# Kernel tuning notes

Measured on AMD Instinct MI355X. Metric: run time of the kernel, lower is better.

## Reference

```python
import jax, jax.numpy as jnp
import numpy as np

B, N, H, V, STEP = 16, 50, 128, 40000, 2

def setup_inputs() -> dict:
    key = jax.random.key(0)
    ks = jax.random.split(key, 24)
    def nrm(i, shape, s=0.08):
        return jax.random.normal(ks[i], shape, jnp.float32) * s
    items = jax.random.randint(ks[0], (B, N), 0, V)
    A = jax.random.uniform(ks[1], (B, N, 2 * N), jnp.float32)
    lengths = jax.random.randint(ks[2], (B,), 1, N + 1)
    mask = (jnp.arange(N)[None, :] < lengths[:, None]).astype(jnp.int32)
    emb = nrm(3, (V, H), 0.1).at[0].set(0.0)  # padding_idx=0 row zeroed
    return dict(
        items=items, A=A, mask=mask, emb=emb,
        w_ih=nrm(4, (3 * H, 2 * H)), w_hh=nrm(5, (3 * H, H)),
        b_ih=nrm(6, (3 * H,)), b_hh=nrm(7, (3 * H,)),
        b_iah=nrm(8, (H,)), b_oah=nrm(9, (H,)),
        W_ein=nrm(10, (H, H)), b_ein=nrm(11, (H,)),
        W_eout=nrm(12, (H, H)), b_eout=nrm(13, (H,)),
        W_one=nrm(14, (H, H)), b_one=nrm(15, (H,)),
        W_two=nrm(16, (H, H)), b_two=nrm(17, (H,)),
        w_three=nrm(18, (H,)),
        W_tr=nrm(19, (H, 2 * H)), b_tr=nrm(20, (H,)),
        W_t=nrm(21, (H, H)),
    )

def gnn_cell(A, hidden, w_ih, w_hh, b_ih, b_hh, b_iah, b_oah, W_ein, b_ein, W_eout, b_eout):
    # A: [B,N,2N], hidden: [B,N,H]
    ein = hidden @ W_ein.T + b_ein
    eout = hidden @ W_eout.T + b_eout
    input_in = jnp.einsum('bnm,bmh->bnh', A[:, :, :N], ein) + b_iah
    input_out = jnp.einsum('bnm,bmh->bnh', A[:, :, N:], eout) + b_oah
    inputs = jnp.concatenate([input_in, input_out], axis=-1)  # [B,N,2H]
    gi = inputs @ w_ih.T + b_ih
    gh = hidden @ w_hh.T + b_hh
    i_r, i_i, i_n = jnp.split(gi, 3, axis=-1)
    h_r, h_i, h_n = jnp.split(gh, 3, axis=-1)
    resetgate = jax.nn.sigmoid(i_r + h_r)
    inputgate = jax.nn.sigmoid(i_i + h_i)
    newgate = jnp.tanh(i_n + resetgate * h_n)
    return newgate + inputgate * (hidden - newgate)

def reference(items, A, mask, emb, w_ih, w_hh, b_ih, b_hh, b_iah, b_oah,
              W_ein, b_ein, W_eout, b_eout, W_one, b_one, W_two, b_two,
              w_three, W_tr, b_tr, W_t):
    hidden = emb[items]  # [B,N,H]
    for _ in range(STEP):
        hidden = gnn_cell(A, hidden, w_ih, w_hh, b_ih, b_hh, b_iah, b_oah,
                          W_ein, b_ein, W_eout, b_eout)
    # compute_scores
    lengths = jnp.sum(mask, axis=1)  # all >= 1 by construction
    ht = hidden[jnp.arange(B), lengths - 1]  # [B,H] last valid item
    q1 = (ht @ W_one.T + b_one)[:, None, :]
    q2 = hidden @ W_two.T + b_two
    mexp = mask[..., None].astype(jnp.float32)  # [B,N,1]
    alpha_logits = jax.nn.sigmoid(q1 + q2) @ w_three[:, None]  # [B,N,1]
    alpha = jax.nn.softmax(jnp.where(mexp == 0, -jnp.inf, alpha_logits), axis=1)
    a = jnp.sum(alpha * hidden * mexp, axis=1)  # [B,H]
    a = jnp.concatenate([a, ht], axis=1) @ W_tr.T + b_tr  # hybrid (nonhybrid=False)
    b_emb = emb[1:]  # [V-1,H]
    qt = (hidden * mexp) @ W_t.T  # [B,N,H]
    beta_logits = jnp.einsum('vh,bnh->bvn', b_emb, qt)
    beta_logits = jnp.where(mask[:, None, :] == 0, -jnp.inf, beta_logits)
    beta = jax.nn.softmax(beta_logits, axis=-1)  # [B,V-1,N]
    target = jnp.einsum('bvn,bnh->bvh', beta, qt * mexp)  # [B,V-1,H]
    # scores = sum((a[:,None,:] + target) * b_emb, -1), split to avoid extra buffer
    scores = jnp.einsum('bvh,vh->bv', target, b_emb) + a @ b_emb.T
    return scores  # [B, V-1]
```

## Files before the change

### kernel.cpp

```cpp
#include <hip/hip_runtime.h>

#define BB 16
#define NN 50
#define HH 128
#define VV 40000
#define VO 39999

typedef unsigned short u16;
typedef unsigned int u32;
typedef __attribute__((ext_vector_type(8))) short short8;
typedef __attribute__((ext_vector_type(4))) float f32x4;

#define OFF_HID    0
#define OFF_EIN    102400
#define OFF_EOUT   204800
#define OFF_QTBF   307200
#define OFF_LEN    411648
#define OFF_WIHT   411664
#define OFF_WHHT   509968
#define OFF_WEINT  559120
#define OFF_WEOUTT 575504
#define OFF_WTWOT  591888
#define OFF_WTT    608272
#define OFF_WONET  624656
#define OFF_WTRT   641040

__device__ __forceinline__ float sigm(float x){ return 1.0f/(1.0f+__expf(-x)); }
__device__ __forceinline__ float b2f(u16 u){
  union { u32 i; float f; } c; c.i = ((u32)u) << 16; return c.f;
}
__device__ __forceinline__ u16 f2b(float f){
  union { float f; u32 i; } c; c.f = f;
  u32 u = c.i;
  return (u16)((u + 0x7fffu + ((u >> 16) & 1u)) >> 16);
}
__device__ __forceinline__ int frag_idx(int b, int n, int k){
  int tile = n>>4, vlo = n&15, kc = k>>5, quad = (k>>3)&3, j = k&7;
  return (((b*4+tile)*4+kc)<<9) + ((quad<<4)+vlo)*8 + j;
}

__global__ void k_pre(const int* __restrict__ items, const float* __restrict__ emb,
                      const float* __restrict__ w_ih, const float* __restrict__ w_hh,
                      const float* __restrict__ W_ein, const float* __restrict__ W_eout,
                      const float* __restrict__ W_two, const float* __restrict__ W_t,
                      const float* __restrict__ W_one, const float* __restrict__ W_tr,
                      float* __restrict__ ws){
  int idx = blockIdx.x*256 + threadIdx.x;
  if (idx < 102400){
    int r = idx >> 7, h = idx & 127;
    ws[OFF_HID + idx] = emb[items[r]*128 + h];
  } else if (idx < 200704){
    int i = idx-102400; int k=i/384, j=i-k*384;
    ws[OFF_WIHT + i] = w_ih[j*256 + k];
  } else if (idx < 249856){
    int i = idx-200704; int k=i/384, j=i-k*384;
    ws[OFF_WHHT + i] = w_hh[j*128 + k];
  } else if (idx < 266240){
    int i = idx-249856; int k=i>>7, h=i&127;
    ws[OFF_WEINT + i] = W_ein[h*128 + k];
  } else if (idx < 282624){
    int i = idx-266240; int k=i>>7, h=i&127;
    ws[OFF_WEOUTT + i] = W_eout[h*128 + k];
  } else if (idx < 299008){
    int i = idx-282624; int k=i>>7, h=i&127;
    ws[OFF_WTWOT + i] = W_two[h*128 + k];
  } else if (idx < 315392){
    int i = idx-299008; int k=i>>7, h=i&127;
    ws[OFF_WTT + i] = W_t[h*128 + k];
  } else if (idx < 331776){
    int i = idx-315392; int k=i>>7, h=i&127;
    ws[OFF_WONET + i] = W_one[h*128 + k];
  } else if (idx < 364544){
    int i = idx-331776; int k=i>>7, h=i&127;
    ws[OFF_WTRT + i] = W_tr[h*256 + k];
  }
}

__global__ void __launch_bounds__(256) k_einout(const float* __restrict__ b_ein,
                         const float* __restrict__ b_eout, float* __restrict__ ws){
  __shared__ float hl[256];
  int t = threadIdx.x;
  int r0 = blockIdx.x * 2;
  hl[t] = ws[OFF_HID + r0*128 + t];
  __syncthreads();
  int h = t & 127;
  const float* wT = ws + ((t<128) ? OFF_WEINT : OFF_WEOUTT);
  float bias = ((t<128)? b_ein : b_eout)[h];
  float a0 = bias, a1 = bias;
  for (int k=0;k<128;k+=4){
    float w0 = wT[(k+0)*128+h], w1 = wT[(k+1)*128+h];
    float w2 = wT[(k+2)*128+h], w3 = wT[(k+3)*128+h];
    float4 h0 = *(const float4*)(hl + k);
    float4 h1 = *(const float4*)(hl + 128 + k);
    a0 += h0.x*w0 + h0.y*w1 + h0.z*w2 + h0.w*w3;
    a1 += h1.x*w0 + h1.y*w1 + h1.z*w2 + h1.w*w3;
  }
  float* dst = ws + ((t<128) ? OFF_EIN : OFF_EOUT);
  dst[(r0+0)*128 + h] = a0;
  dst[(r0+1)*128 + h] = a1;
}

__global__ void __launch_bounds__(384) k_cell(const float* __restrict__ A,
                       const float* __restrict__ b_iah, const float* __restrict__ b_oah,
                       const float* __restrict__ b_ih, const float* __restrict__ b_hh,
                       float* __restrict__ ws){
  __shared__ float hidr[4][128];
  __shared__ float arow[4][104];
  __shared__ float inp[4][256];
  __shared__ float gil[4][384];
  __shared__ float ghl[4][384];
  int t = threadIdx.x;
  int tile = blockIdx.x, b = blockIdx.y;
  int n0 = tile*4;
  for (int o=t; o<512; o+=384){
    int r=o>>7, h=o&127, row=n0+r;
    hidr[r][h] = (row<NN) ? ws[OFF_HID + (b*NN+row)*128 + h] : 0.0f;
  }
  for (int o=t; o<416; o+=384){
    int r=o/104, c=o-r*104;
    arow[r][c] = (c<100 && n0+r<NN) ? A[(size_t)(b*NN+n0+r)*100 + c] : 0.0f;
  }
  __syncthreads();
  for (int o=t; o<1024; o+=384){
    int r = o>>8, c8 = o&255;
    int half = (c8 < 128) ? 1 : 0;
    int c = c8 & 127;
    int row = n0 + r;
    float acc = 0.0f;
    if (row < NN){
      acc = half ? b_iah[c] : b_oah[c];
      const float* src = ws + (half?OFF_EIN:OFF_EOUT) + b*6400 + c;
      const float* ar = &arow[r][half?0:50];
      #pragma unroll 5
      for (int m=0;m<50;m++) acc += ar[m] * src[m*128];
    }
    inp[r][c8] = acc;
  }
  __syncthreads();
  {
    int j = t;
    float gi[4], gh[4];
    float bi = b_ih[j], bh = b_hh[j];
    #pragma unroll
    for (int r=0;r<4;r++){ gi[r]=bi; gh[r]=bh; }
    const float* wti = ws + OFF_WIHT;
    const float* wth = ws + OFF_WHHT;
    for (int k=0;k<256;k+=4){
      float w0 = wti[(k+0)*384+j], w1 = wti[(k+1)*384+j];
      float w2 = wti[(k+2)*384+j], w3_ = wti[(k+3)*384+j];
      #pragma unroll
      for (int r=0;r<4;r++){
        float4 iv = *(const float4*)(&inp[r][k]);
        gi[r] += iv.x*w0 + iv.y*w1 + iv.z*w2 + iv.w*w3_;
      }
    }
    for (int k=0;k<128;k+=4){
      float w0 = wth[(k+0)*384+j], w1 = wth[(k+1)*384+j];
      float w2 = wth[(k+2)*384+j], w3_ = wth[(k+3)*384+j];
      #pragma unroll
      for (int r=0;r<4;r++){
        float4 hv = *(const float4*)(&hidr[r][k]);
        gh[r] += hv.x*w0 + hv.y*w1 + hv.z*w2 + hv.w*w3_;
      }
    }
    #pragma unroll
    for (int r=0;r<4;r++){ gil[r][j]=gi[r]; ghl[r][j]=gh[r]; }
  }
  __syncthreads();
  for (int o=t; o<512; o+=384){
    int r=o>>7, h=o&127, row=n0+r;
    if (row<NN){
      float ir_=gil[r][h], ii=gil[r][128+h], inw=gil[r][256+h];
      float hr_=ghl[r][h], hi=ghl[r][128+h], hn=ghl[r][256+h];
      float rg=sigm(ir_+hr_), ig=sigm(ii+hi), ng=tanhf(inw+rg*hn);
      float hv=hidr[r][h];
      ws[OFF_HID + (b*NN+row)*128 + h] = ng + ig*(hv-ng);
    }
  }
}

__global__ void __launch_bounds__(256) k_tail(const int* __restrict__ mask,
                      const float* __restrict__ b_two, const float* __restrict__ b_one,
                      const float* __restrict__ w_three, const float* __restrict__ b_tr,
                      float* __restrict__ ws){
  __shared__ float hl[1024];
  __shared__ float hidL[6400];
  __shared__ float q2l[NN*129];
  __shared__ float q1l[128], w3l[128], htl[128], al[128], alg[64], parts[256];
  __shared__ int slen_s;
  int bx = blockIdx.x, t = threadIdx.x;
  u16* qtbf = (u16*)(ws + OFF_QTBF);
  if (bx < 100){
    int r0 = bx * 8;
    for (int i=0;i<4;i++) hl[t+i*256] = ws[OFF_HID + r0*128 + t + i*256];
    __syncthreads();
    int h = t & 127, g = t >> 7;
    const float* wT = ws + OFF_WTT;
    float acc[4];
    #pragma unroll
    for (int r=0;r<4;r++) acc[r] = 0.0f;
    for (int k4=0;k4<32;k4++){
      int k = k4*4;
      float w0 = wT[(k+0)*128+h], w1 = wT[(k+1)*128+h];
      float w2 = wT[(k+2)*128+h], w3 = wT[(k+3)*128+h];
      #pragma unroll
      for (int r=0;r<4;r++){
        float4 hv = *(const float4*)(hl + (g*4+r)*128 + k);
        acc[r] += hv.x*w0 + hv.y*w1 + hv.z*w2 + hv.w*w3;
      }
    }
    #pragma unroll
    for (int r=0;r<4;r++){
      int row = r0 + g*4 + r;
      float val = mask[row] ? acc[r] : 0.0f;
      int b = row/NN, n = row - b*NN;
      qtbf[frag_idx(b, n, h)] = f2b(val);
    }
  } else if (bx < 148){
    int i = (bx-100)*256 + t;
    #pragma unroll
    for (int kk=0;kk<2;kk++){
      int e = i*2 + kk;
      int b = e/1536, rem = e - b*1536;
      int kc = rem/384, rem2 = rem - kc*384;
      int quad = rem2/96, vv = rem2 - quad*96;
      int vlo = 4 + vv/8, j = vv & 7;
      qtbf[(((b*4+3)*4+kc)<<9) + ((quad<<4)+vlo)*8 + j] = 0;
    }
  } else {
    int b = bx - 148;
    for (int o=t; o<6400; o+=256) hidL[o] = ws[OFF_HID + b*6400 + o];
    if (t == 0){
      int len = 0;
      for (int n=0;n<NN;n++) len += mask[b*NN+n];
      if (len<1) len=1; if (len>NN) len=NN;
      slen_s = len;
      ((int*)(ws+OFF_LEN))[b] = len;
    }
    __syncthreads();
    int len = slen_s;
    if (t < 128){
      htl[t] = hidL[(len-1)*128 + t];
      w3l[t] = w_three[t];
    }
    __syncthreads();
    if (t < 128){
      const float* w1T = ws + OFF_WONET;
      float q1 = b_one[t];
      for (int k=0;k<128;k++) q1 += htl[k] * w1T[k*128 + t];
      q1l[t] = q1;
    }
    {
      int c = t & 127, g = t >> 7;
      const float* w2T = ws + OFF_WTWOT;
      float bt2 = b_two[c];
      for (int m=g; m<NN; m+=2){
        float acc = bt2;
        const float* hr = hidL + m*128;
        for (int k=0;k<128;k+=4){
          float4 hv = *(const float4*)(hr + k);
          acc += hv.x*w2T[(k+0)*128+c] + hv.y*w2T[(k+1)*128+c]
               + hv.z*w2T[(k+2)*128+c] + hv.w*w2T[(k+3)*128+c];
        }
        q2l[m*129 + c] = acc;
      }
    }
    __syncthreads();
    if (t < 200){
      int r = t>>2, p = t&3;
      float s = 0.0f;
      const float* qr = q2l + r*129;
      for (int h=p*32; h<p*32+32; h++) s += w3l[h]*sigm(q1l[h]+qr[h]);
      parts[t] = s;
    }
    __syncthreads();
    if (t < NN) alg[t] = parts[t*4]+parts[t*4+1]+parts[t*4+2]+parts[t*4+3];
    __syncthreads();
    if (t == 0){
      float mx = -1e30f;
      for (int n=0;n<len;n++) mx = fmaxf(mx, alg[n]);
      float ssum = 0.0f;
      for (int n=0;n<len;n++){ float e=__expf(alg[n]-mx); alg[n]=e; ssum+=e; }
      float inv = (ssum>0.0f)?1.0f/ssum:0.0f;
      for (int n=0;n<len;n++) alg[n]*=inv;
    }
    __syncthreads();
    if (t < 128){
      float a = 0.0f;
      for (int n=0;n<len;n++) a += alg[n]*hidL[n*128+t];
      al[t] = a;
    }
    __syncthreads();
    if (t < 128){
      const float* wtr = ws + OFF_WTRT;
      float af = b_tr[t];
      for (int k=0;k<128;k++) af += al[k]  * wtr[k*128 + t];
      for (int k=0;k<128;k++) af += htl[k] * wtr[(128+k)*128 + t];
      u16 hi = f2b(af);
      u16 lo = f2b(af - b2f(hi));
      qtbf[frag_idx(b, 50, t)] = hi;
      qtbf[frag_idx(b, 51, t)] = lo;
    }
  }
}

__global__ void __launch_bounds__(256) k_scores(const float* __restrict__ emb,
                                                const float* __restrict__ ws,
                                                float* __restrict__ out){
  __shared__ u16 qlds[8192];
  int tid = threadIdx.x;
  int lane = tid & 63, wave = tid >> 6;
  int quad = lane >> 4, vlo = lane & 15;
  int v = blockIdx.y*64 + wave*16 + vlo;
  int vc = (v < VO) ? v : (VO-1);
  const float* erow = emb + (size_t)(vc+1)*128;
  short8 bfr[4];
  #pragma unroll
  for (int kc=0;kc<4;kc++){
    const float4* p = (const float4*)(erow + kc*32 + quad*8);
    float4 x = p[0], y = p[1];
    union { short8 s; u32 w[4]; } u;
    u.w[0] = (u32)f2b(x.x) | ((u32)f2b(x.y)<<16);
    u.w[1] = (u32)f2b(x.z) | ((u32)f2b(x.w)<<16);
    u.w[2] = (u32)f2b(y.x) | ((u32)f2b(y.y)<<16);
    u.w[3] = (u32)f2b(y.z) | ((u32)f2b(y.w)<<16);
    bfr[kc] = u.s;
  }
  const u16* qtf = (const u16*)(ws + OFF_QTBF);
  const int* slen = (const int*)(ws + OFF_LEN);
  int b0 = blockIdx.x*4;
  for (int bi=0;bi<4;bi++){
    int b = b0 + bi;
    __syncthreads();
    {
      const uint4* src = (const uint4*)qtf + (size_t)b*1024;
      uint4* dst = (uint4*)qlds;
      #pragma unroll
      for (int r=0;r<4;r++) dst[tid + r*256] = src[tid + r*256];
    }
    __syncthreads();
    int len = slen[b];
    f32x4 acc0={0.f,0.f,0.f,0.f}, acc1=acc0, acc2=acc0, acc3=acc0;
    #pragma unroll
    for (int kc=0;kc<4;kc++){
      const u16* base = qlds + kc*512 + lane*8;
      short8 a0 = *(const short8*)(base + 0*2048);
      short8 a1 = *(const short8*)(base + 1*2048);
      short8 a2 = *(const short8*)(base + 2*2048);
      short8 a3 = *(const short8*)(base + 3*2048);
      acc0 = __builtin_amdgcn_mfma_f32_16x16x32_bf16(a0, bfr[kc], acc0, 0,0,0);
      acc1 = __builtin_amdgcn_mfma_f32_16x16x32_bf16(a1, bfr[kc], acc1, 0,0,0);
      acc2 = __builtin_amdgcn_mfma_f32_16x16x32_bf16(a2, bfr[kc], acc2, 0,0,0);
      acc3 = __builtin_amdgcn_mfma_f32_16x16x32_bf16(a3, bfr[kc], acc3, 0,0,0);
    }
    int nb = quad*4;
    float ss=0.f, nm=0.f;
    #pragma unroll
    for (int r=0;r<4;r++){
      { int n=nb+r;    if(n<len){ float e=__expf(acc0[r]); ss+=e; nm+=e*acc0[r]; } }
      { int n=nb+r+16; if(n<len){ float e=__expf(acc1[r]); ss+=e; nm+=e*acc1[r]; } }
      { int n=nb+r+32; if(n<len){ float e=__expf(acc2[r]); ss+=e; nm+=e*acc2[r]; } }
      { int n=nb+r+48; if(n<len){ float e=__expf(acc3[r]); ss+=e; nm+=e*acc3[r]; } }
    }
    ss += __shfl_xor(ss,16); ss += __shfl_xor(ss,32);
    nm += __shfl_xor(nm,16); nm += __shfl_xor(nm,32);
    if (quad==0 && v < VO){
      float pa = acc3[2] + acc3[3];
      out[(size_t)b*VO + v] = nm/ss + pa;
    }
  }
}

extern "C" void kernel_launch(void* const* d_in, const int* in_sizes, int n_in,
                              void* d_out, int out_size, void* d_ws, size_t ws_size,
                              hipStream_t stream){
  const int*   items  = (const int*)d_in[0];
  const float* A      = (const float*)d_in[1];
  const int*   mask   = (const int*)d_in[2];
  const float* emb    = (const float*)d_in[3];
  const float* w_ih   = (const float*)d_in[4];
  const float* w_hh   = (const float*)d_in[5];
  const float* b_ih   = (const float*)d_in[6];
  const float* b_hh   = (const float*)d_in[7];
  const float* b_iah  = (const float*)d_in[8];
  const float* b_oah  = (const float*)d_in[9];
  const float* W_ein  = (const float*)d_in[10];
  const float* b_ein  = (const float*)d_in[11];
  const float* W_eout = (const float*)d_in[12];
  const float* b_eout = (const float*)d_in[13];
  const float* W_one  = (const float*)d_in[14];
  const float* b_one  = (const float*)d_in[15];
  const float* W_two  = (const float*)d_in[16];
  const float* b_two  = (const float*)d_in[17];
  const float* w_three= (const float*)d_in[18];
  const float* W_tr   = (const float*)d_in[19];
  const float* b_tr   = (const float*)d_in[20];
  const float* W_t    = (const float*)d_in[21];
  float* ws  = (float*)d_ws;
  float* out = (float*)d_out;

  k_pre<<<1424,256,0,stream>>>(items,emb,w_ih,w_hh,W_ein,W_eout,W_two,W_t,W_one,W_tr,ws);
  for (int s=0;s<2;s++){
    k_einout<<<400,256,0,stream>>>(b_ein,b_eout,ws);
    k_cell  <<<dim3(13,16),384,0,stream>>>(A,b_iah,b_oah,b_ih,b_hh,ws);
  }
  k_tail<<<164,256,0,stream>>>(mask,b_two,b_one,w_three,b_tr,ws);
  k_scores<<<dim3(4,625),256,0,stream>>>(emb,ws,out);
}
```

Before: 228.5 us.

## Fuse edge projections and tail projections into GNN cell kernel via reassociation

Removes the separate k_einout launches by reassociating A·(hW^T+b) into (A·h)W^T + rowsum(A)·b, computed inside the cell kernel from the full batch hidden tile loaded into shared memory. Hidden state is ping-ponged between two buffers so blocks never read rows that another block is overwriting. The second cell step also computes the qt (W_t) and q2 (W_two) projections for its rows, and the qt padding zeroing moves into k_pre. A slim per-batch attention kernel then handles the rest. This cuts launches and global round-trips, at the cost of each cell block redundantly loading all 50 hidden rows and more work per block.

```diff
diff --git a/kernel.cpp b/kernel.cpp
--- a/kernel.cpp
+++ b/kernel.cpp
@@ -12,18 +12,18 @@
 typedef __attribute__((ext_vector_type(4))) float f32x4;
 
 #define OFF_HID    0
-#define OFF_EIN    102400
-#define OFF_EOUT   204800
-#define OFF_QTBF   307200
-#define OFF_LEN    411648
-#define OFF_WIHT   411664
-#define OFF_WHHT   509968
-#define OFF_WEINT  559120
-#define OFF_WEOUTT 575504
-#define OFF_WTWOT  591888
-#define OFF_WTT    608272
-#define OFF_WONET  624656
-#define OFF_WTRT   641040
+#define OFF_HIDB   102400
+#define OFF_Q2     204800
+#define OFF_LEN    307200
+#define OFF_QTBF   307264
+#define OFF_WIHT   372800
+#define OFF_WHHT   471104
+#define OFF_WEINT  520256
+#define OFF_WEOUTT 536640
+#define OFF_WTWOT  553024
+#define OFF_WTT    569408
+#define OFF_WONET  585792
+#define OFF_WTRT   602176
 
 __device__ __forceinline__ float sigm(float x){ return 1.0f/(1.0f+__expf(-x)); }
 __device__ __forceinline__ float b2f(u16 u){
@@ -73,66 +73,77 @@
   } else if (idx < 364544){
     int i = idx-331776; int k=i>>7, h=i&127;
     ws[OFF_WTRT + i] = W_tr[h*256 + k];
-  }
-}
-
-__global__ void __launch_bounds__(256) k_einout(const float* __restrict__ b_ein,
-                         const float* __restrict__ b_eout, float* __restrict__ ws){
-  __shared__ float hl[256];
-  int t = threadIdx.x;
-  int r0 = blockIdx.x * 2;
-  hl[t] = ws[OFF_HID + r0*128 + t];
-  __syncthreads();
-  int h = t & 127;
-  const float* wT = ws + ((t<128) ? OFF_WEINT : OFF_WEOUTT);
-  float bias = ((t<128)? b_ein : b_eout)[h];
-  float a0 = bias, a1 = bias;
-  for (int k=0;k<128;k+=4){
-    float w0 = wT[(k+0)*128+h], w1 = wT[(k+1)*128+h];
-    float w2 = wT[(k+2)*128+h], w3 = wT[(k+3)*128+h];
-    float4 h0 = *(const float4*)(hl + k);
-    float4 h1 = *(const float4*)(hl + 128 + k);
-    a0 += h0.x*w0 + h0.y*w1 + h0.z*w2 + h0.w*w3;
-    a1 += h1.x*w0 + h1.y*w1 + h1.z*w2 + h1.w*w3;
-  }
-  float* dst = ws + ((t<128) ? OFF_EIN : OFF_EOUT);
-  dst[(r0+0)*128 + h] = a0;
-  dst[(r0+1)*128 + h] = a1;
-}
-
-__global__ void __launch_bounds__(384) k_cell(const float* __restrict__ A,
+  } else {
+    u16* qtbf = (u16*)(ws + OFF_QTBF);
+    int i = idx-364544;
+    #pragma unroll
+    for (int kk=0;kk<2;kk++){
+      int e = i*2 + kk;
+      int b = e/1536, rem = e - b*1536;
+      int kc = rem/384, rem2 = rem - kc*384;
+      int quad = rem2/96, vv = rem2 - quad*96;
+      int vlo = 4 + vv/8, j = vv & 7;
+      qtbf[(((b*4+3)*4+kc)<<9) + ((quad<<4)+vlo)*8 + j] = 0;
+    }
+  }
+}
+
+__global__ void __launch_bounds__(384) k_cell2(const float* __restrict__ A,
+                       const int* __restrict__ mask,
                        const float* __restrict__ b_iah, const float* __restrict__ b_oah,
+                       const float* __restrict__ b_ein, const float* __restrict__ b_eout,
                        const float* __restrict__ b_ih, const float* __restrict__ b_hh,
-                       float* __restrict__ ws){
-  __shared__ float hidr[4][128];
+                       const float* __restrict__ b_two,
+                       float* __restrict__ ws, int src_off, int dst_off, int tail){
+  __shared__ float hidL[6400];
   __shared__ float arow[4][104];
+  __shared__ float sAL[4][2];
+  __shared__ float pin[8][128];
   __shared__ float inp[4][256];
   __shared__ float gil[4][384];
   __shared__ float ghl[4][384];
+  __shared__ float hidnew[4][128];
   int t = threadIdx.x;
   int tile = blockIdx.x, b = blockIdx.y;
   int n0 = tile*4;
-  for (int o=t; o<512; o+=384){
-    int r=o>>7, h=o&127, row=n0+r;
-    hidr[r][h] = (row<NN) ? ws[OFF_HID + (b*NN+row)*128 + h] : 0.0f;
-  }
-  for (int o=t; o<416; o+=384){
+  const float* hsrc = ws + src_off + b*6400;
+  for (int o=t;o<6400;o+=384) hidL[o] = hsrc[o];
+  for (int o=t;o<416;o+=384){
     int r=o/104, c=o-r*104;
     arow[r][c] = (c<100 && n0+r<NN) ? A[(size_t)(b*NN+n0+r)*100 + c] : 0.0f;
   }
   __syncthreads();
-  for (int o=t; o<1024; o+=384){
+  if (t<8){
+    int r=t>>1, half=t&1;
+    float s=0.f;
+    for (int m=0;m<50;m++) s += arow[r][half*50+m];
+    sAL[r][half]=s;
+  }
+  for (int o=t;o<1024;o+=384){
+    int pi = o>>7, d = o&127;
+    int r = pi&3, half = pi>>2;
+    float acc = 0.f;
+    const float* ar = &arow[r][half*50];
+    #pragma unroll 5
+    for (int m=0;m<50;m++) acc += ar[m]*hidL[m*128+d];
+    pin[pi][d] = acc;
+  }
+  __syncthreads();
+  for (int o=t;o<1024;o+=384){
     int r = o>>8, c8 = o&255;
-    int half = (c8 < 128) ? 1 : 0;
+    int isin = (c8 < 128) ? 1 : 0;
     int c = c8 & 127;
     int row = n0 + r;
-    float acc = 0.0f;
+    float acc = 0.f;
     if (row < NN){
-      acc = half ? b_iah[c] : b_oah[c];
-      const float* src = ws + (half?OFF_EIN:OFF_EOUT) + b*6400 + c;
-      const float* ar = &arow[r][half?0:50];
-      #pragma unroll 5
-      for (int m=0;m<50;m++) acc += ar[m] * src[m*128];
+      acc = isin ? (b_iah[c] + sAL[r][0]*b_ein[c]) : (b_oah[c] + sAL[r][1]*b_eout[c]);
+      const float* wT = ws + (isin?OFF_WEINT:OFF_WEOUTT);
+      const float* pr = pin[(isin?0:4)+r];
+      for (int d=0;d<128;d+=4){
+        float4 p = *(const float4*)(pr + d);
+        acc += p.x*wT[(d+0)*128+c] + p.y*wT[(d+1)*128+c]
+             + p.z*wT[(d+2)*128+c] + p.w*wT[(d+3)*128+c];
+      }
     }
     inp[r][c8] = acc;
   }
@@ -159,7 +170,7 @@
       float w2 = wth[(k+2)*384+j], w3_ = wth[(k+3)*384+j];
       #pragma unroll
       for (int r=0;r<4;r++){
-        float4 hv = *(const float4*)(&hidr[r][k]);
+        float4 hv = *(const float4*)(&hidL[(n0+r)*128+k]);
         gh[r] += hv.x*w0 + hv.y*w1 + hv.z*w2 + hv.w*w3_;
       }
     }
@@ -167,140 +178,116 @@
     for (int r=0;r<4;r++){ gil[r][j]=gi[r]; ghl[r][j]=gh[r]; }
   }
   __syncthreads();
-  for (int o=t; o<512; o+=384){
+  for (int o=t;o<512;o+=384){
     int r=o>>7, h=o&127, row=n0+r;
     if (row<NN){
       float ir_=gil[r][h], ii=gil[r][128+h], inw=gil[r][256+h];
       float hr_=ghl[r][h], hi=ghl[r][128+h], hn=ghl[r][256+h];
       float rg=sigm(ir_+hr_), ig=sigm(ii+hi), ng=tanhf(inw+rg*hn);
-      float hv=hidr[r][h];
-      ws[OFF_HID + (b*NN+row)*128 + h] = ng + ig*(hv-ng);
-    }
-  }
-}
-
-__global__ void __launch_bounds__(256) k_tail(const int* __restrict__ mask,
-                      const float* __restrict__ b_two, const float* __restrict__ b_one,
-                      const float* __restrict__ w_three, const float* __restrict__ b_tr,
-                      float* __restrict__ ws){
-  __shared__ float hl[1024];
-  __shared__ float hidL[6400];
+      float hv=hidL[row*128+h];
+      float hnew = ng + ig*(hv-ng);
+      ws[dst_off + (b*NN+row)*128 + h] = hnew;
+      hidnew[r][h] = hnew;
+    }
+  }
+  if (!tail) return;
+  __syncthreads();
+  u16* qtbf = (u16*)(ws + OFF_QTBF);
+  for (int o=t;o<1024;o+=384){
+    int kind = o>>9, rem = o&511, r = rem>>7, h = rem&127;
+    int row = n0 + r;
+    if (row < NN){
+      const float* hr = hidnew[r];
+      if (kind==0){
+        float val = 0.f;
+        if (mask[b*NN+row]){
+          const float* wT = ws + OFF_WTT;
+          for (int k=0;k<128;k+=4){
+            float4 hv = *(const float4*)(hr + k);
+            val += hv.x*wT[(k+0)*128+h] + hv.y*wT[(k+1)*128+h]
+                 + hv.z*wT[(k+2)*128+h] + hv.w*wT[(k+3)*128+h];
+          }
+        }
+        qtbf[frag_idx(b, row, h)] = f2b(val);
+      } else {
+        const float* wT = ws + OFF_WTWOT;
+        float acc = b_two[h];
+        for (int k=0;k<128;k+=4){
+          float4 hv = *(const float4*)(hr + k);
+          acc += hv.x*wT[(k+0)*128+h] + hv.y*wT[(k+1)*128+h]
+               + hv.z*wT[(k+2)*128+h] + hv.w*wT[(k+3)*128+h];
+        }
+        ws[OFF_Q2 + (b*NN+row)*128 + h] = acc;
+      }
+    }
+  }
+}
+
+__global__ void __launch_bounds__(256) k_attn2b(const int* __restrict__ mask,
+                        const float* __restrict__ b_one, const float* __restrict__ w_three,
+                        const float* __restrict__ b_tr, float* __restrict__ ws){
   __shared__ float q2l[NN*129];
   __shared__ float q1l[128], w3l[128], htl[128], al[128], alg[64], parts[256];
-  __shared__ int slen_s;
-  int bx = blockIdx.x, t = threadIdx.x;
-  u16* qtbf = (u16*)(ws + OFF_QTBF);
-  if (bx < 100){
-    int r0 = bx * 8;
-    for (int i=0;i<4;i++) hl[t+i*256] = ws[OFF_HID + r0*128 + t + i*256];
-    __syncthreads();
-    int h = t & 127, g = t >> 7;
-    const float* wT = ws + OFF_WTT;
-    float acc[4];
-    #pragma unroll
-    for (int r=0;r<4;r++) acc[r] = 0.0f;
-    for (int k4=0;k4<32;k4++){
-      int k = k4*4;
-      float w0 = wT[(k+0)*128+h], w1 = wT[(k+1)*128+h];
-      float w2 = wT[(k+2)*128+h], w3 = wT[(k+3)*128+h];
-      #pragma unroll
-      for (int r=0;r<4;r++){
-        float4 hv = *(const float4*)(hl + (g*4+r)*128 + k);
-        acc[r] += hv.x*w0 + hv.y*w1 + hv.z*w2 + hv.w*w3;
-      }
-    }
-    #pragma unroll
-    for (int r=0;r<4;r++){
-      int row = r0 + g*4 + r;
-      float val = mask[row] ? acc[r] : 0.0f;
-      int b = row/NN, n = row - b*NN;
-      qtbf[frag_idx(b, n, h)] = f2b(val);
-    }
-  } else if (bx < 148){
-    int i = (bx-100)*256 + t;
-    #pragma unroll
-    for (int kk=0;kk<2;kk++){
-      int e = i*2 + kk;
-      int b = e/1536, rem = e - b*1536;
-      int kc = rem/384, rem2 = rem - kc*384;
-      int quad = rem2/96, vv = rem2 - quad*96;
-      int vlo = 4 + vv/8, j = vv & 7;
-      qtbf[(((b*4+3)*4+kc)<<9) + ((quad<<4)+vlo)*8 + j] = 0;
-    }
-  } else {
-    int b = bx - 148;
-    for (int o=t; o<6400; o+=256) hidL[o] = ws[OFF_HID + b*6400 + o];
-    if (t == 0){
-      int len = 0;
-      for (int n=0;n<NN;n++) len += mask[b*NN+n];
-      if (len<1) len=1; if (len>NN) len=NN;
-      slen_s = len;
-      ((int*)(ws+OFF_LEN))[b] = len;
-    }
-    __syncthreads();
-    int len = slen_s;
-    if (t < 128){
-      htl[t] = hidL[(len-1)*128 + t];
-      w3l[t] = w_three[t];
-    }
-    __syncthreads();
-    if (t < 128){
-      const float* w1T = ws + OFF_WONET;
-      float q1 = b_one[t];
-      for (int k=0;k<128;k++) q1 += htl[k] * w1T[k*128 + t];
-      q1l[t] = q1;
-    }
-    {
-      int c = t & 127, g = t >> 7;
-      const float* w2T = ws + OFF_WTWOT;
-      float bt2 = b_two[c];
-      for (int m=g; m<NN; m+=2){
-        float acc = bt2;
-        const float* hr = hidL + m*128;
-        for (int k=0;k<128;k+=4){
-          float4 hv = *(const float4*)(hr + k);
-          acc += hv.x*w2T[(k+0)*128+c] + hv.y*w2T[(k+1)*128+c]
-               + hv.z*w2T[(k+2)*128+c] + hv.w*w2T[(k+3)*128+c];
-        }
-        q2l[m*129 + c] = acc;
-      }
-    }
-    __syncthreads();
-    if (t < 200){
-      int r = t>>2, p = t&3;
-      float s = 0.0f;
-      const float* qr = q2l + r*129;
-      for (int h=p*32; h<p*32+32; h++) s += w3l[h]*sigm(q1l[h]+qr[h]);
-      parts[t] = s;
-    }
-    __syncthreads();
-    if (t < NN) alg[t] = parts[t*4]+parts[t*4+1]+parts[t*4+2]+parts[t*4+3];
-    __syncthreads();
-    if (t == 0){
-      float mx = -1e30f;
-      for (int n=0;n<len;n++) mx = fmaxf(mx, alg[n]);
-      float ssum = 0.0f;
-      for (int n=0;n<len;n++){ float e=__expf(alg[n]-mx); alg[n]=e; ssum+=e; }
-      float inv = (ssum>0.0f)?1.0f/ssum:0.0f;
-      for (int n=0;n<len;n++) alg[n]*=inv;
-    }
-    __syncthreads();
-    if (t < 128){
-      float a = 0.0f;
-      for (int n=0;n<len;n++) a += alg[n]*hidL[n*128+t];
-      al[t] = a;
-    }
-    __syncthreads();
-    if (t < 128){
-      const float* wtr = ws + OFF_WTRT;
-      float af = b_tr[t];
-      for (int k=0;k<128;k++) af += al[k]  * wtr[k*128 + t];
-      for (int k=0;k<128;k++) af += htl[k] * wtr[(128+k)*128 + t];
-      u16 hi = f2b(af);
-      u16 lo = f2b(af - b2f(hi));
-      qtbf[frag_idx(b, 50, t)] = hi;
-      qtbf[frag_idx(b, 51, t)] = lo;
-    }
+  __shared__ int len_s;
+  int t = threadIdx.x, b = blockIdx.x;
+  for (int o=t;o<NN*128;o+=256){ int n=o>>7, h=o&127; q2l[n*129+h] = ws[OFF_Q2 + b*NN*128 + o]; }
+  if (t==0){
+    int len = 0;
+    for (int n=0;n<NN;n++) len += mask[b*NN+n];
+    if (len<1) len=1; if (len>NN) len=NN;
+    len_s = len;
+    ((int*)(ws+OFF_LEN))[b] = len;
+  }
+  __syncthreads();
+  int len = len_s;
+  if (t < 128){
+    htl[t] = ws[OFF_HID + (b*NN + len-1)*128 + t];
+    w3l[t] = w_three[t];
+  }
+  __syncthreads();
+  if (t < 128){
+    const float* w1T = ws + OFF_WONET;
+    float q1 = b_one[t];
+    for (int k=0;k<128;k++) q1 += htl[k] * w1T[k*128 + t];
+    q1l[t] = q1;
+  }
+  __syncthreads();
+  if (t < 200){
+    int r = t>>2, p = t&3;
+    float s = 0.0f;
+    const float* qr = q2l + r*129;
+    for (int h=p*32; h<p*32+32; h++) s += w3l[h]*sigm(q1l[h]+qr[h]);
+    parts[t] = s;
+  }
+  __syncthreads();
+  if (t < NN) alg[t] = parts[t*4]+parts[t*4+1]+parts[t*4+2]+parts[t*4+3];
+  __syncthreads();
+  if (t == 0){
+    float mx = -1e30f;
+    for (int n=0;n<len;n++) mx = fmaxf(mx, alg[n]);
+    float ssum = 0.0f;
+    for (int n=0;n<len;n++){ float e=__expf(alg[n]-mx); alg[n]=e; ssum+=e; }
+    float inv = (ssum>0.0f)?1.0f/ssum:0.0f;
+    for (int n=0;n<len;n++) alg[n]*=inv;
+  }
+  __syncthreads();
+  if (t < 128){
+    const float* hid = ws + OFF_HID + b*NN*128;
+    float a = 0.0f;
+    for (int n=0;n<len;n++) a += alg[n]*hid[n*128+t];
+    al[t] = a;
+  }
+  __syncthreads();
+  if (t < 128){
+    const float* wtr = ws + OFF_WTRT;
+    float af = b_tr[t];
+    for (int k=0;k<128;k++) af += al[k]  * wtr[k*128 + t];
+    for (int k=0;k<128;k++) af += htl[k] * wtr[(128+k)*128 + t];
+    u16 hi = f2b(af);
+    u16 lo = f2b(af - b2f(hi));
+    u16* qtbf = (u16*)(ws + OFF_QTBF);
+    qtbf[frag_idx(b, 50, t)] = hi;
+    qtbf[frag_idx(b, 51, t)] = lo;
   }
 }
 
@@ -399,11 +386,11 @@
   float* ws  = (float*)d_ws;
   float* out = (float*)d_out;
 
-  k_pre<<<1424,256,0,stream>>>(items,emb,w_ih,w_hh,W_ein,W_eout,W_two,W_t,W_one,W_tr,ws);
-  for (int s=0;s<2;s++){
-    k_einout<<<400,256,0,stream>>>(b_ein,b_eout,ws);
-    k_cell  <<<dim3(13,16),384,0,stream>>>(A,b_iah,b_oah,b_ih,b_hh,ws);
-  }
-  k_tail<<<164,256,0,stream>>>(mask,b_two,b_one,w_three,b_tr,ws);
+  k_pre<<<1472,256,0,stream>>>(items,emb,w_ih,w_hh,W_ein,W_eout,W_two,W_t,W_one,W_tr,ws);
+  k_cell2<<<dim3(13,16),384,0,stream>>>(A,mask,b_iah,b_oah,b_ein,b_eout,b_ih,b_hh,b_two,
+                                        ws, OFF_HID, OFF_HIDB, 0);
+  k_cell2<<<dim3(13,16),384,0,stream>>>(A,mask,b_iah,b_oah,b_ein,b_eout,b_ih,b_hh,b_two,
+                                        ws, OFF_HIDB, OFF_HID, 1);
+  k_attn2b<<<16,256,0,stream>>>(mask,b_one,w_three,b_tr,ws);
   k_scores<<<dim3(4,625),256,0,stream>>>(emb,ws,out);
 }
```

Result: slower. 284.3 us (+24.4%).

## Fuse qt and q2 projections into last GNN cell; move pad zeroing to prep

Applied to the files above, without the earlier changes.

The final k_cell launch now computes the W_t projection (written as bf16 fragments) and the W_two projection (written to a new workspace buffer) from the freshly computed hidden rows kept in shared memory. The old k_tail is replaced by a smaller per-batch k_attn2b kernel that only does the attention softmax and readout. Zeroing of the padded fragment region moves into k_pre. This removes a re-read of hidden and the serial per-batch q2 GEMM from the tail. In exchange the last cell kernel does more work per block and the workspace grows.

```diff
diff --git a/kernel.cpp b/kernel.cpp
--- a/kernel.cpp
+++ b/kernel.cpp
@@ -24,6 +24,7 @@
 #define OFF_WTT    608272
 #define OFF_WONET  624656
 #define OFF_WTRT   641040
+#define OFF_Q2     673808
 
 __device__ __forceinline__ float sigm(float x){ return 1.0f/(1.0f+__expf(-x)); }
 __device__ __forceinline__ float b2f(u16 u){
@@ -73,6 +74,18 @@
   } else if (idx < 364544){
     int i = idx-331776; int k=i>>7, h=i&127;
     ws[OFF_WTRT + i] = W_tr[h*256 + k];
+  } else {
+    u16* qtbf = (u16*)(ws + OFF_QTBF);
+    int i = idx-364544;
+    #pragma unroll
+    for (int kk=0;kk<2;kk++){
+      int e = i*2 + kk;
+      int b = e/1536, rem = e - b*1536;
+      int kc = rem/384, rem2 = rem - kc*384;
+      int quad = rem2/96, vv = rem2 - quad*96;
+      int vlo = 4 + vv/8, j = vv & 7;
+      qtbf[(((b*4+3)*4+kc)<<9) + ((quad<<4)+vlo)*8 + j] = 0;
+    }
   }
 }
 
@@ -101,14 +114,17 @@
 }
 
 __global__ void __launch_bounds__(384) k_cell(const float* __restrict__ A,
+                       const int* __restrict__ mask,
                        const float* __restrict__ b_iah, const float* __restrict__ b_oah,
                        const float* __restrict__ b_ih, const float* __restrict__ b_hh,
-                       float* __restrict__ ws){
+                       const float* __restrict__ b_two,
+                       float* __restrict__ ws, int tail){
   __shared__ float hidr[4][128];
   __shared__ float arow[4][104];
   __shared__ float inp[4][256];
   __shared__ float gil[4][384];
   __shared__ float ghl[4][384];
+  __shared__ float hidnew[4][128];
   int t = threadIdx.x;
   int tile = blockIdx.x, b = blockIdx.y;
   int n0 = tile*4;
@@ -174,133 +190,109 @@
       float hr_=ghl[r][h], hi=ghl[r][128+h], hn=ghl[r][256+h];
       float rg=sigm(ir_+hr_), ig=sigm(ii+hi), ng=tanhf(inw+rg*hn);
       float hv=hidr[r][h];
-      ws[OFF_HID + (b*NN+row)*128 + h] = ng + ig*(hv-ng);
-    }
-  }
-}
-
-__global__ void __launch_bounds__(256) k_tail(const int* __restrict__ mask,
-                      const float* __restrict__ b_two, const float* __restrict__ b_one,
-                      const float* __restrict__ w_three, const float* __restrict__ b_tr,
-                      float* __restrict__ ws){
-  __shared__ float hl[1024];
-  __shared__ float hidL[6400];
+      float hnew = ng + ig*(hv-ng);
+      ws[OFF_HID + (b*NN+row)*128 + h] = hnew;
+      hidnew[r][h] = hnew;
+    }
+  }
+  if (!tail) return;
+  __syncthreads();
+  u16* qtbf = (u16*)(ws + OFF_QTBF);
+  for (int o=t; o<1024; o+=384){
+    int kind = o>>9, rem = o&511, r = rem>>7, h = rem&127;
+    int row = n0 + r;
+    if (row < NN){
+      const float* hr = hidnew[r];
+      if (kind==0){
+        float val = 0.f;
+        if (mask[b*NN+row]){
+          const float* wT = ws + OFF_WTT;
+          for (int k=0;k<128;k+=4){
+            float4 hv = *(const float4*)(hr + k);
+            val += hv.x*wT[(k+0)*128+h] + hv.y*wT[(k+1)*128+h]
+                 + hv.z*wT[(k+2)*128+h] + hv.w*wT[(k+3)*128+h];
+          }
+        }
+        qtbf[frag_idx(b, row, h)] = f2b(val);
+      } else {
+        const float* wT = ws + OFF_WTWOT;
+        float acc = b_two[h];
+        for (int k=0;k<128;k+=4){
+          float4 hv = *(const float4*)(hr + k);
+          acc += hv.x*wT[(k+0)*128+h] + hv.y*wT[(k+1)*128+h]
+               + hv.z*wT[(k+2)*128+h] + hv.w*wT[(k+3)*128+h];
+        }
+        ws[OFF_Q2 + (b*NN+row)*128 + h] = acc;
+      }
+    }
+  }
+}
+
+__global__ void __launch_bounds__(256) k_attn2b(const int* __restrict__ mask,
+                        const float* __restrict__ b_one, const float* __restrict__ w_three,
+                        const float* __restrict__ b_tr, float* __restrict__ ws){
   __shared__ float q2l[NN*129];
   __shared__ float q1l[128], w3l[128], htl[128], al[128], alg[64], parts[256];
-  __shared__ int slen_s;
-  int bx = blockIdx.x, t = threadIdx.x;
-  u16* qtbf = (u16*)(ws + OFF_QTBF);
-  if (bx < 100){
-    int r0 = bx * 8;
-    for (int i=0;i<4;i++) hl[t+i*256] = ws[OFF_HID + r0*128 + t + i*256];
-    __syncthreads();
-    int h = t & 127, g = t >> 7;
-    const float* wT = ws + OFF_WTT;
-    float acc[4];
-    #pragma unroll
-    for (int r=0;r<4;r++) acc[r] = 0.0f;
-    for (int k4=0;k4<32;k4++){
-      int k = k4*4;
-      float w0 = wT[(k+0)*128+h], w1 = wT[(k+1)*128+h];
-      float w2 = wT[(k+2)*128+h], w3 = wT[(k+3)*128+h];
-      #pragma unroll
-      for (int r=0;r<4;r++){
-        float4 hv = *(const float4*)(hl + (g*4+r)*128 + k);
-        acc[r] += hv.x*w0 + hv.y*w1 + hv.z*w2 + hv.w*w3;
-      }
-    }
-    #pragma unroll
-    for (int r=0;r<4;r++){
-      int row = r0 + g*4 + r;
-      float val = mask[row] ? acc[r] : 0.0f;
-      int b = row/NN, n = row - b*NN;
-      qtbf[frag_idx(b, n, h)] = f2b(val);
-    }
-  } else if (bx < 148){
-    int i = (bx-100)*256 + t;
-    #pragma unroll
-    for (int kk=0;kk<2;kk++){
-      int e = i*2 + kk;
-      int b = e/1536, rem = e - b*1536;
-      int kc = rem/384, rem2 = rem - kc*384;
-      int quad = rem2/96, vv = rem2 - quad*96;
-      int vlo = 4 + vv/8, j = vv & 7;
-      qtbf[(((b*4+3)*4+kc)<<9) + ((quad<<4)+vlo)*8 + j] = 0;
-    }
-  } else {
-    int b = bx - 148;
-    for (int o=t; o<6400; o+=256) hidL[o] = ws[OFF_HID + b*6400 + o];
-    if (t == 0){
-      int len = 0;
-      for (int n=0;n<NN;n++) len += mask[b*NN+n];
-      if (len<1) len=1; if (len>NN) len=NN;
-      slen_s = len;
-      ((int*)(ws+OFF_LEN))[b] = len;
-    }
-    __syncthreads();
-    int len = slen_s;
-    if (t < 128){
-      htl[t] = hidL[(len-1)*128 + t];
-      w3l[t] = w_three[t];
-    }
-    __syncthreads();
-    if (t < 128){
-      const float* w1T = ws + OFF_WONET;
-      float q1 = b_one[t];
-      for (int k=0;k<128;k++) q1 += htl[k] * w1T[k*128 + t];
-      q1l[t] = q1;
-    }
-    {
-      int c = t & 127, g = t >> 7;
-      const float* w2T = ws + OFF_WTWOT;
-      float bt2 = b_two[c];
-      for (int m=g; m<NN; m+=2){
-        float acc = bt2;
-        const float* hr = hidL + m*128;
-        for (int k=0;k<128;k+=4){
-          float4 hv = *(const float4*)(hr + k);
-          acc += hv.x*w2T[(k+0)*128+c] + hv.y*w2T[(k+1)*128+c]
-               + hv.z*w2T[(k+2)*128+c] + hv.w*w2T[(k+3)*128+c];
-        }
-        q2l[m*129 + c] = acc;
-      }
-    }
-    __syncthreads();
-    if (t < 200){
-      int r = t>>2, p = t&3;
-      float s = 0.0f;
-      const float* qr = q2l + r*129;
-      for (int h=p*32; h<p*32+32; h++) s += w3l[h]*sigm(q1l[h]+qr[h]);
-      parts[t] = s;
-    }
-    __syncthreads();
-    if (t < NN) alg[t] = parts[t*4]+parts[t*4+1]+parts[t*4+2]+parts[t*4+3];
-    __syncthreads();
-    if (t == 0){
-      float mx = -1e30f;
-      for (int n=0;n<len;n++) mx = fmaxf(mx, alg[n]);
-      float ssum = 0.0f;
-      for (int n=0;n<len;n++){ float e=__expf(alg[n]-mx); alg[n]=e; ssum+=e; }
-      float inv = (ssum>0.0f)?1.0f/ssum:0.0f;
-      for (int n=0;n<len;n++) alg[n]*=inv;
-    }
-    __syncthreads();
-    if (t < 128){
-      float a = 0.0f;
-      for (int n=0;n<len;n++) a += alg[n]*hidL[n*128+t];
-      al[t] = a;
-    }
-    __syncthreads();
-    if (t < 128){
-      const float* wtr = ws + OFF_WTRT;
-      float af = b_tr[t];
-      for (int k=0;k<128;k++) af += al[k]  * wtr[k*128 + t];
-      for (int k=0;k<128;k++) af += htl[k] * wtr[(128+k)*128 + t];
-      u16 hi = f2b(af);
-      u16 lo = f2b(af - b2f(hi));
-      qtbf[frag_idx(b, 50, t)] = hi;
-      qtbf[frag_idx(b, 51, t)] = lo;
-    }
+  __shared__ int len_s;
+  int t = threadIdx.x, b = blockIdx.x;
+  for (int o=t;o<NN*128;o+=256){ int n=o>>7, h=o&127; q2l[n*129+h] = ws[OFF_Q2 + b*NN*128 + o]; }
+  if (t==0){
+    int len = 0;
+    for (int n=0;n<NN;n++) len += mask[b*NN+n];
+    if (len<1) len=1; if (len>NN) len=NN;
+    len_s = len;
+    ((int*)(ws+OFF_LEN))[b] = len;
+  }
+  __syncthreads();
+  int len = len_s;
+  if (t < 128){
+    htl[t] = ws[OFF_HID + (b*NN + len-1)*128 + t];
+    w3l[t] = w_three[t];
+  }
+  __syncthreads();
+  if (t < 128){
+    const float* w1T = ws + OFF_WONET;
+    float q1 = b_one[t];
+    for (int k=0;k<128;k++) q1 += htl[k] * w1T[k*128 + t];
+    q1l[t] = q1;
+  }
+  __syncthreads();
+  if (t < 200){
+    int r = t>>2, p = t&3;
+    float s = 0.0f;
+    const float* qr = q2l + r*129;
+    for (int h=p*32; h<p*32+32; h++) s += w3l[h]*sigm(q1l[h]+qr[h]);
+    parts[t] = s;
+  }
+  __syncthreads();
+  if (t < NN) alg[t] = parts[t*4]+parts[t*4+1]+parts[t*4+2]+parts[t*4+3];
+  __syncthreads();
+  if (t == 0){
+    float mx = -1e30f;
+    for (int n=0;n<len;n++) mx = fmaxf(mx, alg[n]);
+    float ssum = 0.0f;
+    for (int n=0;n<len;n++){ float e=__expf(alg[n]-mx); alg[n]=e; ssum+=e; }
+    float inv = (ssum>0.0f)?1.0f/ssum:0.0f;
+    for (int n=0;n<len;n++) alg[n]*=inv;
+  }
+  __syncthreads();
+  if (t < 128){
+    const float* hid = ws + OFF_HID + b*NN*128;
+    float a = 0.0f;
+    for (int n=0;n<len;n++) a += alg[n]*hid[n*128+t];
+    al[t] = a;
+  }
+  __syncthreads();
+  if (t < 128){
+    const float* wtr = ws + OFF_WTRT;
+    float af = b_tr[t];
+    for (int k=0;k<128;k++) af += al[k]  * wtr[k*128 + t];
+    for (int k=0;k<128;k++) af += htl[k] * wtr[(128+k)*128 + t];
+    u16 hi = f2b(af);
+    u16 lo = f2b(af - b2f(hi));
+    u16* qtbf = (u16*)(ws + OFF_QTBF);
+    qtbf[frag_idx(b, 50, t)] = hi;
+    qtbf[frag_idx(b, 51, t)] = lo;
   }
 }
 
@@ -399,11 +391,11 @@
   float* ws  = (float*)d_ws;
   float* out = (float*)d_out;
 
-  k_pre<<<1424,256,0,stream>>>(items,emb,w_ih,w_hh,W_ein,W_eout,W_two,W_t,W_one,W_tr,ws);
-  for (int s=0;s<2;s++){
-    k_einout<<<400,256,0,stream>>>(b_ein,b_eout,ws);
-    k_cell  <<<dim3(13,16),384,0,stream>>>(A,b_iah,b_oah,b_ih,b_hh,ws);
-  }
-  k_tail<<<164,256,0,stream>>>(mask,b_two,b_one,w_three,b_tr,ws);
+  k_pre<<<1472,256,0,stream>>>(items,emb,w_ih,w_hh,W_ein,W_eout,W_two,W_t,W_one,W_tr,ws);
+  k_einout<<<400,256,0,stream>>>(b_ein,b_eout,ws);
+  k_cell  <<<dim3(13,16),384,0,stream>>>(A,mask,b_iah,b_oah,b_ih,b_hh,b_two,ws,0);
+  k_einout<<<400,256,0,stream>>>(b_ein,b_eout,ws);
+  k_cell  <<<dim3(13,16),384,0,stream>>>(A,mask,b_iah,b_oah,b_ih,b_hh,b_two,ws,1);
+  k_attn2b<<<16,256,0,stream>>>(mask,b_one,w_three,b_tr,ws);
   k_scores<<<dim3(4,625),256,0,stream>>>(emb,ws,out);
 }
```

Result: slower. 279.0 us (+22.1%).
